# Performance work log

Hardware: AMD Instinct MI355X
Metric: run time of the kernel (lower is better)

The kernel has to match this reference:

```python
import jax, jax.numpy as jnp
import numpy as np

LOG2 = 0.6931471805599453

def ssp(x):
    # shifted softplus: softplus(x) - log(2)
    return jax.nn.softplus(x) - LOG2

def residual(v, W, b):
    # PhysNetResidual reuses the same linear twice: linear(act(linear(act(x)))) + x
    h = ssp(v) @ W + b
    h = ssp(h) @ W + b
    return h + v

def setup_inputs() -> dict:
    key = jax.random.key(0)
    ks = jax.random.split(key, 20)
    N, E, D, R = 50000, 600000, 128, 32
    n_int, n_atom_res, n_out_res = 3, 1, 1
    def orth(k, shape):
        return jax.random.orthogonal(k, shape[0])[: shape[0], : shape[1]].astype(jnp.float32) if shape[0] == shape[1] else jax.random.normal(k, shape, jnp.float32) * (1.0 / np.sqrt(shape[0]))
    return {
        "x": jax.random.normal(ks[0], (N, D), jnp.float32),
        "g_ij": jax.random.uniform(ks[1], (E, R), jnp.float32),
        "Wf": orth(ks[2], (D, D)), "bf": jnp.zeros((D,), jnp.float32),
        "Wg": jax.random.normal(ks[3], (R, D), jnp.float32) * (1.0 / np.sqrt(R)),
        "Wj": orth(ks[4], (D, D)), "bj": jnp.zeros((D,), jnp.float32),
        "Wi": orth(ks[5], (D, D)), "bi": jnp.zeros((D,), jnp.float32),
        "u": jnp.ones((D,), jnp.float32),
        "rWint": jnp.stack([orth(ks[6 + i], (D, D)) for i in range(n_int)]),
        "rbint": jnp.zeros((n_int, D), jnp.float32),
        "rWatom": jnp.stack([orth(ks[10 + i], (D, D)) for i in range(n_atom_res)]),
        "rbatom": jnp.zeros((n_atom_res, D), jnp.float32),
        "rWout": jnp.stack([orth(ks[12 + i], (D, D)) for i in range(n_out_res)]),
        "rbout": jnp.zeros((n_out_res, D), jnp.float32),
        "idx_i": jax.random.randint(ks[14], (E,), 0, N, jnp.int32),
        "idx_j": jax.random.randint(ks[15], (E,), 0, N, jnp.int32),
        "n_atoms": N,
    }

def reference(x, g_ij, Wf, bf, Wg, Wj, bj, Wi, bi, u,
              rWint, rbint, rWatom, rbatom, rWout, rbout,
              idx_i, idx_j, n_atoms):
    # --- PhysNetInteraction ---
    xa = ssp(x)                                   # [N, D]
    x_j = xa[idx_j]                               # gather -> [E, D]
    xp = u * xa                                   # [N, D]
    vp = ssp(x_j @ Wj + bj) * (g_ij @ Wg)         # [E, D] RBF-gated messages
    vm = ssp(xa @ Wi + bi)                        # [N, D]
    v = jax.ops.segment_sum(vp, idx_i, num_segments=n_atoms) + vm
    for k in range(rWint.shape[0]):
        v = residual(v, rWint[k], rbint[k])
    v = ssp(v)
    h = xp + v @ Wf + bf                          # [N, D]
    # --- atomic residual stack ---
    for k in range(rWatom.shape[0]):
        h = residual(h, rWatom[k], rbatom[k])
    # --- PhysNetOutput ---
    o = h
    for k in range(rWout.shape[0]):
        o = residual(o, rWout[k], rbout[k])
    o = ssp(o)
    return (o, h)
```

## Files before the change

kernel.cpp:

```cpp
#include <hip/hip_runtime.h>
#include <stdint.h>

#define LOG2F 0.693147180559945f

typedef __attribute__((ext_vector_type(8))) short short8;
typedef __attribute__((ext_vector_type(4))) float f32x4;

__device__ __forceinline__ float ssp(float x){
  float t = __expf(-fabsf(x));
  return fmaxf(x, 0.0f) + __logf(1.0f + t) - LOG2F;
}

__device__ __forceinline__ uint32_t bf16rn(float x){
  uint32_t u = __float_as_uint(x);
  return (u + 0x7fffu + ((u >> 16) & 1u)) >> 16;
}
__device__ __forceinline__ void split2(float x, unsigned short &h, unsigned short &l){
  uint32_t hb = bf16rn(x);
  h = (unsigned short)hb;
  float hf = __uint_as_float(hb << 16);
  l = (unsigned short)bf16rn(x - hf);
}


__global__ __launch_bounds__(256) void k_xconv(
    const float* __restrict__ x, unsigned short* __restrict__ xs, int total)
{
  int i = (blockIdx.x * 256 + threadIdx.x) * 4;
  if (i >= total) return;
  int row = i >> 7, col = i & 127;
  float4 f4 = *(const float4*)(x + i);
  ushort4 h4, l4;
  split2(ssp(f4.x), h4.x, l4.x);
  split2(ssp(f4.y), h4.y, l4.y);
  split2(ssp(f4.z), h4.z, l4.z);
  split2(ssp(f4.w), h4.w, l4.w);
  *(ushort4*)(xs + (size_t)row * 256 + col)       = h4;
  *(ushort4*)(xs + (size_t)row * 256 + 128 + col) = l4;
}

__global__ __launch_bounds__(256) void k_hist(
    const int* __restrict__ idx_i, int* __restrict__ cnt, int E)
{
  int e = blockIdx.x * 256 + threadIdx.x;
  if (e < E) atomicAdd(&cnt[idx_i[e]], 1);
}

__global__ __launch_bounds__(256) void k_scan1(
    int* __restrict__ cnt, int* __restrict__ bsums, int N)
{
  __shared__ int sh[256];
  const int t = threadIdx.x;
  const int base = blockIdx.x * 2048 + t * 8;
  int loc[8], s = 0;
#pragma unroll
  for (int k = 0; k < 8; ++k){
    int v = (base + k < N) ? cnt[base + k] : 0;
    loc[k] = s; s += v;
  }
  sh[t] = s;
  __syncthreads();
  const int own = s;
  for (int off = 1; off < 256; off <<= 1){
    int v = (t >= off) ? sh[t - off] : 0;
    __syncthreads();
    sh[t] += v;
    __syncthreads();
  }
  const int ex = sh[t] - own;
#pragma unroll
  for (int k = 0; k < 8; ++k)
    if (base + k < N) cnt[base + k] = ex + loc[k];
  if (t == 255) bsums[blockIdx.x] = sh[255];
}

__global__ void k_scan2(int* __restrict__ bsums, int nblk){
  if (threadIdx.x == 0 && blockIdx.x == 0){
    int run = 0;
    for (int b = 0; b < nblk; ++b){ int v = bsums[b]; bsums[b] = run; run += v; }
  }
}

__global__ __launch_bounds__(256) void k_scan3(
    int* __restrict__ cnt, const int* __restrict__ bsums, int N)
{
  int i = blockIdx.x * 256 + threadIdx.x;
  if (i < N) cnt[i] += bsums[i >> 11];
}

__global__ __launch_bounds__(256) void k_scatter(
    const int* __restrict__ idx_i, int* __restrict__ ofs,
    int* __restrict__ perm, int E)
{
  int e = blockIdx.x * 256 + threadIdx.x;
  if (e < E){
    int p = atomicAdd(&ofs[idx_i[e]], 1);
    perm[p] = e;
  }
}

__global__ __launch_bounds__(256) void k_wconv(
    const float* __restrict__ Wj, const float* __restrict__ Wg,
    const float* __restrict__ Wi, const float* __restrict__ Wf,
    const float* __restrict__ Wint, const float* __restrict__ Watm,
    const float* __restrict__ Wout,
    unsigned short* __restrict__ ws, int ni, int na, int no)
{
  const int nmat = 3 + ni + na + no;
  int t = blockIdx.x * 256 + threadIdx.x;
  int m = t >> 11, r = t & 2047;
  if (m < nmat){
    const float* src;
    if      (m == 0)           src = Wj;
    else if (m == 1)           src = Wi;
    else if (m <= 1 + ni)      src = Wint + (size_t)(m - 2) * 16384;
    else if (m == 2 + ni)      src = Wf;
    else if (m <= 2 + ni + na) src = Watm + (size_t)(m - 3 - ni) * 16384;
    else                       src = Wout + (size_t)(m - 3 - ni - na) * 16384;
    int lane = r & 63, s = (r >> 6) & 3, ct = r >> 8;
    int col = ct * 16 + (lane & 15);
    int k0  = s * 32 + (lane >> 4) * 8;
    union { unsigned short u[8]; uint4 v; } H, L;
#pragma unroll
    for (int i = 0; i < 8; ++i) split2(src[(size_t)(k0 + i) * 128 + col], H.u[i], L.u[i]);
    ((uint4*)ws)[(size_t)m * 4096 + ((ct * 4 + s) * 2 + 0) * 64 + lane] = H.v;
    ((uint4*)ws)[(size_t)m * 4096 + ((ct * 4 + s) * 2 + 1) * 64 + lane] = L.v;
  } else {
    int uu = t - nmat * 2048;
    if (uu < 512){
      int lane = uu & 63, ct = uu >> 6;
      int col = ct * 16 + (lane & 15);
      int k0  = (lane >> 4) * 8;
      union { unsigned short u8[8]; uint4 v; } H, L;
#pragma unroll
      for (int i = 0; i < 8; ++i) split2(Wg[(size_t)(k0 + i) * 128 + col], H.u8[i], L.u8[i]);
      ((uint4*)ws)[(size_t)nmat * 4096 + (ct * 2 + 0) * 64 + lane] = H.v;
      ((uint4*)ws)[(size_t)nmat * 4096 + (ct * 2 + 1) * 64 + lane] = L.v;
    }
  }
}

__global__ __launch_bounds__(256) void k_edge(
    const unsigned short* __restrict__ xs, const float* __restrict__ g,
    const int* __restrict__ idx_i, const int* __restrict__ idx_j,
    const int* __restrict__ perm,
    const short8* __restrict__ wjf, const short8* __restrict__ wgf,
    const float* __restrict__ bj, float* vacc, int E)
{
  __shared__ __align__(16) char smem[16384 + 4096];
  short8* ahl = (short8*)smem;
  short8* ghl = (short8*)(smem + 16384);
  float*  vp_s = (float*)smem;
  __shared__ int ii_s[32];

  const int t    = threadIdx.x;
  const int lane = t & 63;
  const int w    = t >> 6;
  const int l15  = lane & 15;
  const int lq   = lane >> 4;
  const int e0   = blockIdx.x * 32;

  {
    const int row = t >> 3, kseg = t & 7;
    const int pe = e0 + row;
    const int e = (pe < E) ? perm[pe] : 0;
    const int j = idx_j[e];
    const short8* xp = (const short8*)(xs + (size_t)j * 256);
    const int q0 = kseg * 2;
    short8 fh0 = xp[q0    ];
    short8 fh1 = xp[q0 + 1];
    short8 fl0 = xp[16 + q0    ];
    short8 fl1 = xp[16 + q0 + 1];
    ahl[0*512 + (q0+0)*32 + (row ^ (q0+0))] = fh0;
    ahl[0*512 + (q0+1)*32 + (row ^ (q0+1))] = fh1;
    ahl[1*512 + (q0+0)*32 + (row ^ (q0+0))] = fl0;
    ahl[1*512 + (q0+1)*32 + (row ^ (q0+1))] = fl1;
  }
  if (t < 64){
    const int row = t >> 1, kseg = t & 1;
    const int pe = e0 + row;
    const int e = (pe < E) ? perm[pe] : 0;
    const float4* gp = (const float4*)(g + (size_t)e * 32 + kseg * 16);
    short8 fh0, fh1, fl0, fl1;
#pragma unroll
    for (int q = 0; q < 4; ++q){
      float4 f4 = gp[q];
      float vv[4] = {f4.x, f4.y, f4.z, f4.w};
#pragma unroll
      for (int uu = 0; uu < 4; ++uu){
        unsigned short hh, ll;
        split2(vv[uu], hh, ll);
        int i = q * 4 + uu;
        if (i < 8){ fh0[i]   = (short)hh; fl0[i]   = (short)ll; }
        else      { fh1[i-8] = (short)hh; fl1[i-8] = (short)ll; }
      }
    }
    const int q0 = kseg * 2;
    ghl[0*128 + (q0+0)*32 + (row ^ (q0+0))] = fh0;
    ghl[0*128 + (q0+1)*32 + (row ^ (q0+1))] = fh1;
    ghl[1*128 + (q0+0)*32 + (row ^ (q0+0))] = fl0;
    ghl[1*128 + (q0+1)*32 + (row ^ (q0+1))] = fl1;
  }
  if (t >= 64 && t < 96){
    int rr = t - 64, pe = e0 + rr;
    ii_s[rr] = (pe < E) ? idx_i[perm[pe]] : -1;
  }
  __syncthreads();

  f32x4 am[2][2], ag[2][2];
#pragma unroll
  for (int a = 0; a < 2; ++a)
#pragma unroll
    for (int b = 0; b < 2; ++b){
      am[a][b] = (f32x4){0.f, 0.f, 0.f, 0.f};
      ag[a][b] = (f32x4){0.f, 0.f, 0.f, 0.f};
    }

#pragma unroll
  for (int s = 0; s < 4; ++s){
    const int q = s * 4 + lq;
    short8 a0h = ahl[0*512 + q*32 + ((l15     ) ^ q)];
    short8 a0l = ahl[1*512 + q*32 + ((l15     ) ^ q)];
    short8 a1h = ahl[0*512 + q*32 + ((16 + l15) ^ q)];
    short8 a1l = ahl[1*512 + q*32 + ((16 + l15) ^ q)];
#pragma unroll
    for (int c = 0; c < 2; ++c){
      const int ct = w * 2 + c;
      short8 bh = wjf[((ct*4 + s)*2 + 0)*64 + lane];
      short8 bl = wjf[((ct*4 + s)*2 + 1)*64 + lane];
      am[0][c] = __builtin_amdgcn_mfma_f32_16x16x32_bf16(a0h, bh, am[0][c], 0, 0, 0);
      am[0][c] = __builtin_amdgcn_mfma_f32_16x16x32_bf16(a0h, bl, am[0][c], 0, 0, 0);
      am[0][c] = __builtin_amdgcn_mfma_f32_16x16x32_bf16(a0l, bh, am[0][c], 0, 0, 0);
      am[1][c] = __builtin_amdgcn_mfma_f32_16x16x32_bf16(a1h, bh, am[1][c], 0, 0, 0);
      am[1][c] = __builtin_amdgcn_mfma_f32_16x16x32_bf16(a1h, bl, am[1][c], 0, 0, 0);
      am[1][c] = __builtin_amdgcn_mfma_f32_16x16x32_bf16(a1l, bh, am[1][c], 0, 0, 0);
    }
  }
  {
    const int q = lq;
    short8 g0h = ghl[0*128 + q*32 + ((l15     ) ^ q)];
    short8 g0l = ghl[1*128 + q*32 + ((l15     ) ^ q)];
    short8 g1h = ghl[0*128 + q*32 + ((16 + l15) ^ q)];
    short8 g1l = ghl[1*128 + q*32 + ((16 + l15) ^ q)];
#pragma unroll
    for (int c = 0; c < 2; ++c){
      const int ct = w * 2 + c;
      short8 bh = wgf[(ct*2 + 0)*64 + lane];
      short8 bl = wgf[(ct*2 + 1)*64 + lane];
      ag[0][c] = __builtin_amdgcn_mfma_f32_16x16x32_bf16(g0h, bh, ag[0][c], 0, 0, 0);
      ag[0][c] = __builtin_amdgcn_mfma_f32_16x16x32_bf16(g0h, bl, ag[0][c], 0, 0, 0);
      ag[0][c] = __builtin_amdgcn_mfma_f32_16x16x32_bf16(g0l, bh, ag[0][c], 0, 0, 0);
      ag[1][c] = __builtin_amdgcn_mfma_f32_16x16x32_bf16(g1h, bh, ag[1][c], 0, 0, 0);
      ag[1][c] = __builtin_amdgcn_mfma_f32_16x16x32_bf16(g1h, bl, ag[1][c], 0, 0, 0);
      ag[1][c] = __builtin_amdgcn_mfma_f32_16x16x32_bf16(g1l, bh, ag[1][c], 0, 0, 0);
    }
  }

  __syncthreads();
#pragma unroll
  for (int c = 0; c < 2; ++c){
    const int col = (w * 2 + c) * 16 + l15;
    const float bjv = bj[col];
#pragma unroll
    for (int rt = 0; rt < 2; ++rt)
#pragma unroll
      for (int r = 0; r < 4; ++r){
        const int row = rt * 16 + lq * 4 + r;
        vp_s[col * 33 + row] = ssp(am[rt][c][r] + bjv) * ag[rt][c][r];
      }
  }
  __syncthreads();
  {
    const int col = t & 127;
    const int rbase = (t >> 7) * 16;
    float acc = 0.f;
    int curi = -1;
#pragma unroll
    for (int r = 0; r < 16; ++r){
      const int ii = ii_s[rbase + r];
      const float v = vp_s[col * 33 + rbase + r];
      if (ii == curi) acc += v;
      else {
        if (curi >= 0) atomicAdd(&vacc[(size_t)curi * 128 + col], acc);
        acc = v; curi = ii;
      }
    }
    if (curi >= 0) atomicAdd(&vacc[(size_t)curi * 128 + col], acc);
  }
}

__global__ __launch_bounds__(256) void k_chain(
    const float* __restrict__ x, const float* vacc,
    const short8* __restrict__ wcf,
    const float* __restrict__ bi, const float* __restrict__ bf_,
    const float* __restrict__ u,
    const float* __restrict__ bint, const float* __restrict__ batm,
    const float* __restrict__ bout,
    float* out, int N, int ni, int na, int no)
{
  __shared__ short8 ahl[2][1024];

  const int t    = threadIdx.x;
  const int lane = t & 63;
  const int w    = t >> 6;
  const int l15  = lane & 15;
  const int lq   = lane >> 4;
  const int r0   = blockIdx.x * 32;

  const int col0 = (w*2 + 0)*16 + l15;
  const int col1 = (w*2 + 1)*16 + l15;
  const int q0c = col0 >> 3, e0c = col0 & 7;
  const int q1c = col1 >> 3, e1c = col1 & 7;

  f32x4 am[2][2];
  int cur = 0;

  auto frag_put = [&](int b, int row, int qc, int ec, float v){
    unsigned short hh, ll;
    split2(v, hh, ll);
    unsigned short* base = (unsigned short*)&ahl[b][0];
    const int idx = (qc*32 + (row ^ qc))*8 + ec;
    base[idx]        = hh;
    base[4096 + idx] = ll;
  };

  auto gemm = [&](const short8* __restrict__ wf){
    const short8* A = &ahl[cur][0];
#pragma unroll
    for (int a = 0; a < 2; ++a)
#pragma unroll
      for (int b = 0; b < 2; ++b) am[a][b] = (f32x4){0.f, 0.f, 0.f, 0.f};
#pragma unroll
    for (int s = 0; s < 4; ++s){
      const int q = s * 4 + lq;
      short8 a0h = A[0*512 + q*32 + ((l15     ) ^ q)];
      short8 a0l = A[1*512 + q*32 + ((l15     ) ^ q)];
      short8 a1h = A[0*512 + q*32 + ((16 + l15) ^ q)];
      short8 a1l = A[1*512 + q*32 + ((16 + l15) ^ q)];
#pragma unroll
      for (int c = 0; c < 2; ++c){
        const int ct = w * 2 + c;
        short8 bh = wf[((ct*4 + s)*2 + 0)*64 + lane];
        short8 bl = wf[((ct*4 + s)*2 + 1)*64 + lane];
        am[0][c] = __builtin_amdgcn_mfma_f32_16x16x32_bf16(a0h, bh, am[0][c], 0, 0, 0);
        am[0][c] = __builtin_amdgcn_mfma_f32_16x16x32_bf16(a0h, bl, am[0][c], 0, 0, 0);
        am[0][c] = __builtin_amdgcn_mfma_f32_16x16x32_bf16(a0l, bh, am[0][c], 0, 0, 0);
        am[1][c] = __builtin_amdgcn_mfma_f32_16x16x32_bf16(a1h, bh, am[1][c], 0, 0, 0);
        am[1][c] = __builtin_amdgcn_mfma_f32_16x16x32_bf16(a1h, bl, am[1][c], 0, 0, 0);
        am[1][c] = __builtin_amdgcn_mfma_f32_16x16x32_bf16(a1l, bh, am[1][c], 0, 0, 0);
      }
    }
  };

  auto put_ssp_state = [&](float (&st)[2][2][4]){
    const int b = cur ^ 1;
#pragma unroll
    for (int rt = 0; rt < 2; ++rt)
#pragma unroll
      for (int r = 0; r < 4; ++r){
        const int row = rt*16 + lq*4 + r;
        frag_put(b, row, q0c, e0c, ssp(st[rt][0][r]));
        frag_put(b, row, q1c, e1c, ssp(st[rt][1][r]));
      }
    __syncthreads();
    cur = b;
  };
  auto put_ssp_amb = [&](float b0, float b1){
    const int b = cur ^ 1;
#pragma unroll
    for (int rt = 0; rt < 2; ++rt)
#pragma unroll
      for (int r = 0; r < 4; ++r){
        const int row = rt*16 + lq*4 + r;
        frag_put(b, row, q0c, e0c, ssp(am[rt][0][r] + b0));
        frag_put(b, row, q1c, e1c, ssp(am[rt][1][r] + b1));
      }
    __syncthreads();
    cur = b;
  };

  auto residual = [&](float (&st)[2][2][4], const short8* wf, const float* bvec){
    const float b0 = bvec[col0], b1 = bvec[col1];
    put_ssp_state(st);
    gemm(wf);
    put_ssp_amb(b0, b1);
    gemm(wf);
#pragma unroll
    for (int rt = 0; rt < 2; ++rt)
#pragma unroll
      for (int r = 0; r < 4; ++r){
        st[rt][0][r] += am[rt][0][r] + b0;
        st[rt][1][r] += am[rt][1][r] + b1;
      }
  };

  float xar[2][2][4];
#pragma unroll
  for (int rt = 0; rt < 2; ++rt)
#pragma unroll
    for (int r = 0; r < 4; ++r){
      int row = r0 + rt*16 + lq*4 + r; if (row >= N) row = N - 1;
      const int lrow = rt*16 + lq*4 + r;
      float v0 = ssp(x[(size_t)row*128 + col0]);
      float v1 = ssp(x[(size_t)row*128 + col1]);
      xar[rt][0][r] = v0; xar[rt][1][r] = v1;
      frag_put(0, lrow, q0c, e0c, v0);
      frag_put(0, lrow, q1c, e1c, v1);
    }
  __syncthreads();

  gemm(wcf + 0);
  float vst[2][2][4];
  {
    const float b0 = bi[col0], b1 = bi[col1];
#pragma unroll
    for (int rt = 0; rt < 2; ++rt)
#pragma unroll
      for (int r = 0; r < 4; ++r){
        int row = r0 + rt*16 + lq*4 + r; if (row >= N) row = N - 1;
        vst[rt][0][r] = vacc[(size_t)row*128 + col0] + ssp(am[rt][0][r] + b0);
        vst[rt][1][r] = vacc[(size_t)row*128 + col1] + ssp(am[rt][1][r] + b1);
      }
  }

  for (int kk = 0; kk < ni; ++kk)
    residual(vst, wcf + (size_t)(1 + kk) * 4096, bint + kk*128);

  put_ssp_state(vst);
  gemm(wcf + (size_t)(1 + ni) * 4096);
  float hst[2][2][4];
  {
    const float b0 = bf_[col0], b1 = bf_[col1];
    const float u0 = u[col0],   u1 = u[col1];
#pragma unroll
    for (int rt = 0; rt < 2; ++rt)
#pragma unroll
      for (int r = 0; r < 4; ++r){
        hst[rt][0][r] = u0 * xar[rt][0][r] + am[rt][0][r] + b0;
        hst[rt][1][r] = u1 * xar[rt][1][r] + am[rt][1][r] + b1;
      }
  }

  for (int kk = 0; kk < na; ++kk)
    residual(hst, wcf + (size_t)(2 + ni + kk) * 4096, batm + kk*128);

#pragma unroll
  for (int rt = 0; rt < 2; ++rt)
#pragma unroll
    for (int r = 0; r < 4; ++r){
      const int row = r0 + rt*16 + lq*4 + r;
      if (row < N){
        out[(size_t)N*128 + (size_t)row*128 + col0] = hst[rt][0][r];
        out[(size_t)N*128 + (size_t)row*128 + col1] = hst[rt][1][r];
      }
    }

  for (int kk = 0; kk < no; ++kk)
    residual(hst, wcf + (size_t)(2 + ni + na + kk) * 4096, bout + kk*128);

#pragma unroll
  for (int rt = 0; rt < 2; ++rt)
#pragma unroll
    for (int r = 0; r < 4; ++r){
      const int row = r0 + rt*16 + lq*4 + r;
      if (row < N){
        out[(size_t)row*128 + col0] = ssp(hst[rt][0][r]);
        out[(size_t)row*128 + col1] = ssp(hst[rt][1][r]);
      }
    }
}

extern "C" void kernel_launch(void* const* d_in, const int* in_sizes, int n_in,
                              void* d_out, int out_size, void* d_ws, size_t ws_size,
                              hipStream_t stream)
{
  const float* x    = (const float*)d_in[0];
  const float* g    = (const float*)d_in[1];
  const float* Wf   = (const float*)d_in[2];
  const float* bf_  = (const float*)d_in[3];
  const float* Wg   = (const float*)d_in[4];
  const float* Wj   = (const float*)d_in[5];
  const float* bj   = (const float*)d_in[6];
  const float* Wi   = (const float*)d_in[7];
  const float* bi   = (const float*)d_in[8];
  const float* u    = (const float*)d_in[9];
  const float* Wint = (const float*)d_in[10];
  const float* bint = (const float*)d_in[11];
  const float* Watm = (const float*)d_in[12];
  const float* batm = (const float*)d_in[13];
  const float* Wout = (const float*)d_in[14];
  const float* bout = (const float*)d_in[15];
  const int* idx_i  = (const int*)d_in[16];
  const int* idx_j  = (const int*)d_in[17];

  const int N  = in_sizes[0] / 128;
  const int E  = in_sizes[16];
  const int ni = in_sizes[10] / 16384;
  const int na = in_sizes[12] / 16384;
  const int no = in_sizes[14] / 16384;

  const int nmat = 3 + ni + na + no;

  float* vacc = (float*)d_out;
  short8* wsf = (short8*)d_ws;
  const short8* wjf = wsf;
  const short8* wcf = wsf + (size_t)1 * 4096;
  const short8* wgf = wsf + (size_t)nmat * 4096;

  const size_t frag_bytes = (size_t)(nmat + 1) * 65536;
  int* cnt   = (int*)((char*)d_ws + frag_bytes);
  int* bsums = cnt + N;
  int* perm  = bsums + 1024;
  char* after = (char*)(perm + E);
  const size_t used = (size_t)(after - (char*)d_ws);
  const size_t xs_bytes = (size_t)N * 256 * sizeof(unsigned short);
  unsigned short* xs = (ws_size >= used + xs_bytes)
      ? (unsigned short*)after
      : (unsigned short*)((float*)d_out + (size_t)N * 128);

  const int nblk = (N + 2047) / 2048;

  hipMemsetAsync(vacc, 0, (size_t)N * 128 * sizeof(float), stream);
  hipMemsetAsync(cnt, 0, (size_t)N * sizeof(int), stream);
  k_xconv  <<<dim3((N*128/4 + 255)/256), dim3(256), 0, stream>>>(x, xs, N * 128);
  k_wconv  <<<dim3((nmat + 1) * 8), dim3(256), 0, stream>>>(Wj, Wg, Wi, Wf, Wint, Watm, Wout,
                                                            (unsigned short*)d_ws, ni, na, no);
  k_hist   <<<dim3((E + 255)/256), dim3(256), 0, stream>>>(idx_i, cnt, E);
  k_scan1  <<<dim3(nblk), dim3(256), 0, stream>>>(cnt, bsums, N);
  k_scan2  <<<dim3(1), dim3(64), 0, stream>>>(bsums, nblk);
  k_scan3  <<<dim3((N + 255)/256), dim3(256), 0, stream>>>(cnt, bsums, N);
  k_scatter<<<dim3((E + 255)/256), dim3(256), 0, stream>>>(idx_i, cnt, perm, E);
  k_edge   <<<dim3((E + 31)/32), dim3(256), 0, stream>>>(xs, g, idx_i, idx_j, perm,
                                                         wjf, wgf, bj, vacc, E);
  k_chain  <<<dim3((N + 31)/32), dim3(256), 0, stream>>>(x, vacc, wcf,
                                                         bi, bf_, u, bint, batm, bout,
                                                         (float*)d_out, N, ni, na, no);
}
```

Before: 533.4 us.

## Fuse setup kernels and widen k_chain row tile to 64 rows

The two memsets become zero-stores inside k_xconv, the histogram moves into k_wconv as a grid-stride loop, and k_scan3 is dropped by adding the block offset inside k_scatter. Together these remove four launches and a pass over the counts. k_chain now processes 64 rows per block, with each wave owning 32 rows by 64 columns, so weight fragments loaded from global memory are reused across more rows, at the cost of double the LDS and more accumulator registers (launch bounds of 2 blocks per CU). One risk: the histogram in k_wconv may not be ordered after the cnt zeroing in k_xconv, but both run on the same stream, so launch order keeps it correct.

```diff
diff --git a/kernel.cpp b/kernel.cpp
--- a/kernel.cpp
+++ b/kernel.cpp
@@ -24,7 +24,8 @@
 
 
 __global__ __launch_bounds__(256) void k_xconv(
-    const float* __restrict__ x, unsigned short* __restrict__ xs, int total)
+    const float* __restrict__ x, unsigned short* __restrict__ xs,
+    float* __restrict__ vacc, int* __restrict__ cnt, int total)
 {
   int i = (blockIdx.x * 256 + threadIdx.x) * 4;
   if (i >= total) return;
@@ -37,66 +38,8 @@
   split2(ssp(f4.w), h4.w, l4.w);
   *(ushort4*)(xs + (size_t)row * 256 + col)       = h4;
   *(ushort4*)(xs + (size_t)row * 256 + 128 + col) = l4;
-}
-
-__global__ __launch_bounds__(256) void k_hist(
-    const int* __restrict__ idx_i, int* __restrict__ cnt, int E)
-{
-  int e = blockIdx.x * 256 + threadIdx.x;
-  if (e < E) atomicAdd(&cnt[idx_i[e]], 1);
-}
-
-__global__ __launch_bounds__(256) void k_scan1(
-    int* __restrict__ cnt, int* __restrict__ bsums, int N)
-{
-  __shared__ int sh[256];
-  const int t = threadIdx.x;
-  const int base = blockIdx.x * 2048 + t * 8;
-  int loc[8], s = 0;
-#pragma unroll
-  for (int k = 0; k < 8; ++k){
-    int v = (base + k < N) ? cnt[base + k] : 0;
-    loc[k] = s; s += v;
-  }
-  sh[t] = s;
-  __syncthreads();
-  const int own = s;
-  for (int off = 1; off < 256; off <<= 1){
-    int v = (t >= off) ? sh[t - off] : 0;
-    __syncthreads();
-    sh[t] += v;
-    __syncthreads();
-  }
-  const int ex = sh[t] - own;
-#pragma unroll
-  for (int k = 0; k < 8; ++k)
-    if (base + k < N) cnt[base + k] = ex + loc[k];
-  if (t == 255) bsums[blockIdx.x] = sh[255];
-}
-
-__global__ void k_scan2(int* __restrict__ bsums, int nblk){
-  if (threadIdx.x == 0 && blockIdx.x == 0){
-    int run = 0;
-    for (int b = 0; b < nblk; ++b){ int v = bsums[b]; bsums[b] = run; run += v; }
-  }
-}
-
-__global__ __launch_bounds__(256) void k_scan3(
-    int* __restrict__ cnt, const int* __restrict__ bsums, int N)
-{
-  int i = blockIdx.x * 256 + threadIdx.x;
-  if (i < N) cnt[i] += bsums[i >> 11];
-}
-
-__global__ __launch_bounds__(256) void k_scatter(
-    const int* __restrict__ idx_i, int* __restrict__ ofs,
-    int* __restrict__ perm, int E)
-{
-  int e = blockIdx.x * 256 + threadIdx.x;
-  if (e < E){
-    int p = atomicAdd(&ofs[idx_i[e]], 1);
-    perm[p] = e;
-  }
+  *(float4*)(vacc + i) = (float4){0.f, 0.f, 0.f, 0.f};
+  if (col == 0) cnt[row] = 0;
 }
 
 __global__ __launch_bounds__(256) void k_wconv(
@@ -104,7 +47,8 @@
     const float* __restrict__ Wi, const float* __restrict__ Wf,
     const float* __restrict__ Wint, const float* __restrict__ Watm,
     const float* __restrict__ Wout,
-    unsigned short* __restrict__ ws, int ni, int na, int no)
+    unsigned short* __restrict__ ws, int ni, int na, int no,
+    const int* __restrict__ idx_i, int* __restrict__ cnt, int E)
 {
   const int nmat = 3 + ni + na + no;
   int t = blockIdx.x * 256 + threadIdx.x;
@@ -138,6 +82,56 @@
       ((uint4*)ws)[(size_t)nmat * 4096 + (ct * 2 + 1) * 64 + lane] = L.v;
     }
   }
+  const int stride = gridDim.x * 256;
+  for (int e = blockIdx.x * 256 + threadIdx.x; e < E; e += stride)
+    atomicAdd(&cnt[idx_i[e]], 1);
+}
+
+__global__ __launch_bounds__(256) void k_scan1(
+    int* __restrict__ cnt, int* __restrict__ bsums, int N)
+{
+  __shared__ int sh[256];
+  const int t = threadIdx.x;
+  const int base = blockIdx.x * 2048 + t * 8;
+  int loc[8], s = 0;
+#pragma unroll
+  for (int k = 0; k < 8; ++k){
+    int v = (base + k < N) ? cnt[base + k] : 0;
+    loc[k] = s; s += v;
+  }
+  sh[t] = s;
+  __syncthreads();
+  const int own = s;
+  for (int off = 1; off < 256; off <<= 1){
+    int v = (t >= off) ? sh[t - off] : 0;
+    __syncthreads();
+    sh[t] += v;
+    __syncthreads();
+  }
+  const int ex = sh[t] - own;
+#pragma unroll
+  for (int k = 0; k < 8; ++k)
+    if (base + k < N) cnt[base + k] = ex + loc[k];
+  if (t == 255) bsums[blockIdx.x] = sh[255];
+}
+
+__global__ void k_scan2(int* __restrict__ bsums, int nblk){
+  if (threadIdx.x == 0 && blockIdx.x == 0){
+    int run = 0;
+    for (int b = 0; b < nblk; ++b){ int v = bsums[b]; bsums[b] = run; run += v; }
+  }
+}
+
+__global__ __launch_bounds__(256) void k_scatter(
+    const int* __restrict__ idx_i, int* __restrict__ cnt,
+    const int* __restrict__ bsums, int* __restrict__ perm, int E)
+{
+  int e = blockIdx.x * 256 + threadIdx.x;
+  if (e < E){
+    int ii = idx_i[e];
+    int p = atomicAdd(&cnt[ii], 1) + bsums[ii >> 11];
+    perm[p] = e;
+  }
 }
 
 __global__ __launch_bounds__(256) void k_edge(
@@ -289,7 +283,7 @@
   }
 }
 
-__global__ __launch_bounds__(256) void k_chain(
+__global__ __launch_bounds__(256, 2) void k_chain(
     const float* __restrict__ x, const float* vacc,
     const short8* __restrict__ wcf,
     const float* __restrict__ bi, const float* __restrict__ bf_,
@@ -298,30 +292,36 @@
     const float* __restrict__ bout,
     float* out, int N, int ni, int na, int no)
 {
-  __shared__ short8 ahl[2][1024];
+  __shared__ short8 ahl[2][2048];
 
   const int t    = threadIdx.x;
   const int lane = t & 63;
   const int w    = t >> 6;
   const int l15  = lane & 15;
   const int lq   = lane >> 4;
-  const int r0   = blockIdx.x * 32;
-
-  const int col0 = (w*2 + 0)*16 + l15;
-  const int col1 = (w*2 + 1)*16 + l15;
-  const int q0c = col0 >> 3, e0c = col0 & 7;
-  const int q1c = col1 >> 3, e1c = col1 & 7;
-
-  f32x4 am[2][2];
+  const int rh   = w >> 1;
+  const int ch   = w & 1;
+  const int r0   = blockIdx.x * 64;
+  const int rbase = rh * 32;
+
+  int cols[4], qc[4], ec[4];
+#pragma unroll
+  for (int cf = 0; cf < 4; ++cf){
+    cols[cf] = (ch * 4 + cf) * 16 + l15;
+    qc[cf] = cols[cf] >> 3;
+    ec[cf] = cols[cf] & 7;
+  }
+
+  f32x4 am[2][4];
   int cur = 0;
 
-  auto frag_put = [&](int b, int row, int qc, int ec, float v){
+  auto frag_put = [&](int b, int row, int qcv, int ecv, float v){
     unsigned short hh, ll;
     split2(v, hh, ll);
     unsigned short* base = (unsigned short*)&ahl[b][0];
-    const int idx = (qc*32 + (row ^ qc))*8 + ec;
+    const int idx = (qcv*64 + (row ^ qcv))*8 + ecv;
     base[idx]        = hh;
-    base[4096 + idx] = ll;
+    base[8192 + idx] = ll;
   };
 
   auto gemm = [&](const short8* __restrict__ wf){
@@ -329,98 +329,100 @@
 #pragma unroll
     for (int a = 0; a < 2; ++a)
 #pragma unroll
-      for (int b = 0; b < 2; ++b) am[a][b] = (f32x4){0.f, 0.f, 0.f, 0.f};
+      for (int cf = 0; cf < 4; ++cf) am[a][cf] = (f32x4){0.f, 0.f, 0.f, 0.f};
 #pragma unroll
     for (int s = 0; s < 4; ++s){
       const int q = s * 4 + lq;
-      short8 a0h = A[0*512 + q*32 + ((l15     ) ^ q)];
-      short8 a0l = A[1*512 + q*32 + ((l15     ) ^ q)];
-      short8 a1h = A[0*512 + q*32 + ((16 + l15) ^ q)];
-      short8 a1l = A[1*512 + q*32 + ((16 + l15) ^ q)];
-#pragma unroll
-      for (int c = 0; c < 2; ++c){
-        const int ct = w * 2 + c;
+      short8 a0h = A[       q*64 + ((rbase      + l15) ^ q)];
+      short8 a0l = A[1024 + q*64 + ((rbase      + l15) ^ q)];
+      short8 a1h = A[       q*64 + ((rbase + 16 + l15) ^ q)];
+      short8 a1l = A[1024 + q*64 + ((rbase + 16 + l15) ^ q)];
+#pragma unroll
+      for (int cf = 0; cf < 4; ++cf){
+        const int ct = ch * 4 + cf;
         short8 bh = wf[((ct*4 + s)*2 + 0)*64 + lane];
         short8 bl = wf[((ct*4 + s)*2 + 1)*64 + lane];
-        am[0][c] = __builtin_amdgcn_mfma_f32_16x16x32_bf16(a0h, bh, am[0][c], 0, 0, 0);
-        am[0][c] = __builtin_amdgcn_mfma_f32_16x16x32_bf16(a0h, bl, am[0][c], 0, 0, 0);
-        am[0][c] = __builtin_amdgcn_mfma_f32_16x16x32_bf16(a0l, bh, am[0][c], 0, 0, 0);
-        am[1][c] = __builtin_amdgcn_mfma_f32_16x16x32_bf16(a1h, bh, am[1][c], 0, 0, 0);
-        am[1][c] = __builtin_amdgcn_mfma_f32_16x16x32_bf16(a1h, bl, am[1][c], 0, 0, 0);
-        am[1][c] = __builtin_amdgcn_mfma_f32_16x16x32_bf16(a1l, bh, am[1][c], 0, 0, 0);
+        am[0][cf] = __builtin_amdgcn_mfma_f32_16x16x32_bf16(a0h, bh, am[0][cf], 0, 0, 0);
+        am[0][cf] = __builtin_amdgcn_mfma_f32_16x16x32_bf16(a0h, bl, am[0][cf], 0, 0, 0);
+        am[0][cf] = __builtin_amdgcn_mfma_f32_16x16x32_bf16(a0l, bh, am[0][cf], 0, 0, 0);
+        am[1][cf] = __builtin_amdgcn_mfma_f32_16x16x32_bf16(a1h, bh, am[1][cf], 0, 0, 0);
+        am[1][cf] = __builtin_amdgcn_mfma_f32_16x16x32_bf16(a1h, bl, am[1][cf], 0, 0, 0);
+        am[1][cf] = __builtin_amdgcn_mfma_f32_16x16x32_bf16(a1l, bh, am[1][cf], 0, 0, 0);
       }
     }
   };
 
-  auto put_ssp_state = [&](float (&st)[2][2][4]){
+  auto put_ssp_state = [&](float (&st)[2][4][4]){
     const int b = cur ^ 1;
 #pragma unroll
     for (int rt = 0; rt < 2; ++rt)
 #pragma unroll
-      for (int r = 0; r < 4; ++r){
-        const int row = rt*16 + lq*4 + r;
-        frag_put(b, row, q0c, e0c, ssp(st[rt][0][r]));
-        frag_put(b, row, q1c, e1c, ssp(st[rt][1][r]));
-      }
+      for (int cf = 0; cf < 4; ++cf)
+#pragma unroll
+        for (int r = 0; r < 4; ++r)
+          frag_put(b, rbase + rt*16 + lq*4 + r, qc[cf], ec[cf], ssp(st[rt][cf][r]));
     __syncthreads();
     cur = b;
   };
-  auto put_ssp_amb = [&](float b0, float b1){
+  auto put_ssp_amb = [&](const float (&bv)[4]){
     const int b = cur ^ 1;
 #pragma unroll
     for (int rt = 0; rt < 2; ++rt)
 #pragma unroll
-      for (int r = 0; r < 4; ++r){
-        const int row = rt*16 + lq*4 + r;
-        frag_put(b, row, q0c, e0c, ssp(am[rt][0][r] + b0));
-        frag_put(b, row, q1c, e1c, ssp(am[rt][1][r] + b1));
-      }
+      for (int cf = 0; cf < 4; ++cf)
+#pragma unroll
+        for (int r = 0; r < 4; ++r)
+          frag_put(b, rbase + rt*16 + lq*4 + r, qc[cf], ec[cf], ssp(am[rt][cf][r] + bv[cf]));
     __syncthreads();
     cur = b;
   };
 
-  auto residual = [&](float (&st)[2][2][4], const short8* wf, const float* bvec){
-    const float b0 = bvec[col0], b1 = bvec[col1];
+  auto residual = [&](float (&st)[2][4][4], const short8* wf, const float* bvec){
+    float bv[4];
+#pragma unroll
+    for (int cf = 0; cf < 4; ++cf) bv[cf] = bvec[cols[cf]];
     put_ssp_state(st);
     gemm(wf);
-    put_ssp_amb(b0, b1);
+    put_ssp_amb(bv);
     gemm(wf);
 #pragma unroll
     for (int rt = 0; rt < 2; ++rt)
 #pragma unroll
+      for (int cf = 0; cf < 4; ++cf)
+#pragma unroll
+        for (int r = 0; r < 4; ++r)
+          st[rt][cf][r] += am[rt][cf][r] + bv[cf];
+  };
+
+  float xar[2][4][4];
+#pragma unroll
+  for (int rt = 0; rt < 2; ++rt)
+#pragma unroll
+    for (int cf = 0; cf < 4; ++cf)
+#pragma unroll
       for (int r = 0; r < 4; ++r){
-        st[rt][0][r] += am[rt][0][r] + b0;
-        st[rt][1][r] += am[rt][1][r] + b1;
-      }
-  };
-
-  float xar[2][2][4];
-#pragma unroll
-  for (int rt = 0; rt < 2; ++rt)
-#pragma unroll
-    for (int r = 0; r < 4; ++r){
-      int row = r0 + rt*16 + lq*4 + r; if (row >= N) row = N - 1;
-      const int lrow = rt*16 + lq*4 + r;
-      float v0 = ssp(x[(size_t)row*128 + col0]);
-      float v1 = ssp(x[(size_t)row*128 + col1]);
-      xar[rt][0][r] = v0; xar[rt][1][r] = v1;
-      frag_put(0, lrow, q0c, e0c, v0);
-      frag_put(0, lrow, q1c, e1c, v1);
-    }
+        int row = r0 + rbase + rt*16 + lq*4 + r; if (row >= N) row = N - 1;
+        float v = ssp(x[(size_t)row*128 + cols[cf]]);
+        xar[rt][cf][r] = v;
+        frag_put(0, rbase + rt*16 + lq*4 + r, qc[cf], ec[cf], v);
+      }
   __syncthreads();
 
   gemm(wcf + 0);
-  float vst[2][2][4];
+  float vst[2][4][4];
   {
-    const float b0 = bi[col0], b1 = bi[col1];
+    float bv[4];
+#pragma unroll
+    for (int cf = 0; cf < 4; ++cf) bv[cf] = bi[cols[cf]];
 #pragma unroll
     for (int rt = 0; rt < 2; ++rt)
 #pragma unroll
-      for (int r = 0; r < 4; ++r){
-        int row = r0 + rt*16 + lq*4 + r; if (row >= N) row = N - 1;
-        vst[rt][0][r] = vacc[(size_t)row*128 + col0] + ssp(am[rt][0][r] + b0);
-        vst[rt][1][r] = vacc[(size_t)row*128 + col1] + ssp(am[rt][1][r] + b1);
-      }
+      for (int cf = 0; cf < 4; ++cf)
+#pragma unroll
+        for (int r = 0; r < 4; ++r){
+          int row = r0 + rbase + rt*16 + lq*4 + r; if (row >= N) row = N - 1;
+          vst[rt][cf][r] = vacc[(size_t)row*128 + cols[cf]] + ssp(am[rt][cf][r] + bv[cf]);
+        }
   }
 
   for (int kk = 0; kk < ni; ++kk)
@@ -428,17 +430,18 @@
 
   put_ssp_state(vst);
   gemm(wcf + (size_t)(1 + ni) * 4096);
-  float hst[2][2][4];
+  float hst[2][4][4];
   {
-    const float b0 = bf_[col0], b1 = bf_[col1];
-    const float u0 = u[col0],   u1 = u[col1];
+    float bv[4], uv[4];
+#pragma unroll
+    for (int cf = 0; cf < 4; ++cf){ bv[cf] = bf_[cols[cf]]; uv[cf] = u[cols[cf]]; }
 #pragma unroll
     for (int rt = 0; rt < 2; ++rt)
 #pragma unroll
-      for (int r = 0; r < 4; ++r){
-        hst[rt][0][r] = u0 * xar[rt][0][r] + am[rt][0][r] + b0;
-        hst[rt][1][r] = u1 * xar[rt][1][r] + am[rt][1][r] + b1;
-      }
+      for (int cf = 0; cf < 4; ++cf)
+#pragma unroll
+        for (int r = 0; r < 4; ++r)
+          hst[rt][cf][r] = uv[cf] * xar[rt][cf][r] + am[rt][cf][r] + bv[cf];
   }
 
   for (int kk = 0; kk < na; ++kk)
@@ -447,13 +450,12 @@
 #pragma unroll
   for (int rt = 0; rt < 2; ++rt)
 #pragma unroll
-    for (int r = 0; r < 4; ++r){
-      const int row = r0 + rt*16 + lq*4 + r;
-      if (row < N){
-        out[(size_t)N*128 + (size_t)row*128 + col0] = hst[rt][0][r];
-        out[(size_t)N*128 + (size_t)row*128 + col1] = hst[rt][1][r];
-      }
-    }
+    for (int cf = 0; cf < 4; ++cf)
+#pragma unroll
+      for (int r = 0; r < 4; ++r){
+        const int row = r0 + rbase + rt*16 + lq*4 + r;
+        if (row < N) out[(size_t)N*128 + (size_t)row*128 + cols[cf]] = hst[rt][cf][r];
+      }
 
   for (int kk = 0; kk < no; ++kk)
     residual(hst, wcf + (size_t)(2 + ni + na + kk) * 4096, bout + kk*128);
@@ -461,13 +463,12 @@
 #pragma unroll
   for (int rt = 0; rt < 2; ++rt)
 #pragma unroll
-    for (int r = 0; r < 4; ++r){
-      const int row = r0 + rt*16 + lq*4 + r;
-      if (row < N){
-        out[(size_t)row*128 + col0] = ssp(hst[rt][0][r]);
-        out[(size_t)row*128 + col1] = ssp(hst[rt][1][r]);
-      }
-    }
+    for (int cf = 0; cf < 4; ++cf)
+#pragma unroll
+      for (int r = 0; r < 4; ++r){
+        const int row = r0 + rbase + rt*16 + lq*4 + r;
+        if (row < N) out[(size_t)row*128 + cols[cf]] = ssp(hst[rt][cf][r]);
+      }
 }
 
 extern "C" void kernel_launch(void* const* d_in, const int* in_sizes, int n_in,
@@ -520,19 +521,16 @@
 
   const int nblk = (N + 2047) / 2048;
 
-  hipMemsetAsync(vacc, 0, (size_t)N * 128 * sizeof(float), stream);
-  hipMemsetAsync(cnt, 0, (size_t)N * sizeof(int), stream);
-  k_xconv  <<<dim3((N*128/4 + 255)/256), dim3(256), 0, stream>>>(x, xs, N * 128);
+  k_xconv  <<<dim3((N*128/4 + 255)/256), dim3(256), 0, stream>>>(x, xs, vacc, cnt, N * 128);
   k_wconv  <<<dim3((nmat + 1) * 8), dim3(256), 0, stream>>>(Wj, Wg, Wi, Wf, Wint, Watm, Wout,
-                                                            (unsigned short*)d_ws, ni, na, no);
-  k_hist   <<<dim3((E + 255)/256), dim3(256), 0, stream>>>(idx_i, cnt, E);
+                                                            (unsigned short*)d_ws, ni, na, no,
+                                                            idx_i, cnt, E);
   k_scan1  <<<dim3(nblk), dim3(256), 0, stream>>>(cnt, bsums, N);
   k_scan2  <<<dim3(1), dim3(64), 0, stream>>>(bsums, nblk);
-  k_scan3  <<<dim3((N + 255)/256), dim3(256), 0, stream>>>(cnt, bsums, N);
-  k_scatter<<<dim3((E + 255)/256), dim3(256), 0, stream>>>(idx_i, cnt, perm, E);
+  k_scatter<<<dim3((E + 255)/256), dim3(256), 0, stream>>>(idx_i, cnt, bsums, perm, E);
   k_edge   <<<dim3((E + 31)/32), dim3(256), 0, stream>>>(xs, g, idx_i, idx_j, perm,
                                                          wjf, wgf, bj, vacc, E);
-  k_chain  <<<dim3((N + 31)/32), dim3(256), 0, stream>>>(x, vacc, wcf,
+  k_chain  <<<dim3((N + 63)/64), dim3(256), 0, stream>>>(x, vacc, wcf,
                                                          bi, bf_, u, bint, batm, bout,
                                                          (float*)d_out, N, ni, na, no);
 }
```

Measured after the change: 598.3 us. +12.2%, slower.
